# Kernel optimization log

Hardware: AMD Instinct MI355X
Metric: run time of the kernel (lower is better)

## Reference

```python
import jax, jax.numpy as jnp
import numpy as np

H = 64          # hidden_dim
EP = 60000      # edges per relation type; block order: nmos, pmos, R, L, C
E = 5 * EP
N_IN = 50000
N_OUT = 50000


def _gelu(x):
    return jax.nn.gelu(x, approximate=False)  # torch nn.GELU default = exact erf


def _mlp_blocked(x, Ws, bs):
    # x: [T, N, Din]; independent MLP per relation-type block; GELU after all but last layer
    for i, (W, b) in enumerate(zip(Ws, bs)):
        x = jnp.einsum('tnd,tdh->tnh', x, W) + b[:, None, :]
        if i < len(Ws) - 1:
            x = _gelu(x)
    return x


def _mlp(x, Ws, bs):
    for i, (W, b) in enumerate(zip(Ws, bs)):
        x = x @ W + b
        if i < len(Ws) - 1:
            x = _gelu(x)
    return x


def _segment_softmax(logits, seg, num_seg):
    # torch_geometric-style softmax: normalized per dst-node segment, per feature column
    m = jax.ops.segment_max(logits, seg, num_segments=num_seg)
    ex = jnp.exp(logits - m[seg])
    den = jax.ops.segment_sum(ex, seg, num_segments=num_seg)
    return ex / den[seg]


def _forward(floats, src_types, dst_types, src_nodes, dst_nodes,
             vg_types, vg_idx, vb_types, vb_idx, n_output_nodes):
    (input_voltages, device_params, nf1_W, nf1_b,
     ef1_W1, ef1_b1, ef1_W2, ef1_b2, ef1_W3, ef1_b3,
     ef2m_W1, ef2m_b1, ef2m_W2, ef2m_b2, ef2m_W3, ef2m_b3, ef2m_W4, ef2m_b4,
     ef2r_W1, ef2r_b1, ef2r_W2, ef2r_b2, ef2r_W3, ef2r_b3, ef2r_W4, ef2r_b4,
     self_W1, self_b1, self_W2, self_b2, self_W3, self_b3, self_W4, self_b4,
     score_W, score_b) = floats
    # ef1: per-relation-type 3-layer MLP on the scalar device parameter -> [E, H]
    ef1 = _mlp_blocked(device_params,
                       [ef1_W1, ef1_W2, ef1_W3],
                       [ef1_b1, ef1_b2, ef1_b3]).reshape(E, H)
    nf1_input = input_voltages[:, None] @ nf1_W + nf1_b           # [N_IN, H]
    # (ef1 @ ef1.T)[dst_out] @ ef1 == ef1[dst_out] @ (ef1.T @ ef1) -- avoids the E x E matrix
    logits = ef1 @ (ef1.T @ ef1)                                  # [E, H]
    # edges whose dst is not an 'output' node go to a dump segment that is dropped
    seg = jnp.where(dst_types == 1, dst_nodes, n_output_nodes)
    att = _segment_softmax(logits, seg, n_output_nodes + 1)
    nf1_output = jax.ops.segment_sum(att * ef1, seg,
                                     num_segments=n_output_nodes + 1)[:n_output_nodes]

    def pick(types, idx):
        # node_types.index: 0 -> 'input' table, 1 -> 'output' table
        return jnp.where((types == 0)[:, None], nf1_input[idx], nf1_output[idx])

    nf1_src = pick(src_types, src_nodes)
    nf1_dst = pick(dst_types, dst_nodes)
    nf1_vg = pick(vg_types, vg_idx)     # gate node feats (mos edges only) [2*EP, H]
    nf1_vb = pick(vb_types, vb_idx)     # bulk node feats (mos edges only) [2*EP, H]

    M = 2 * EP
    x_mos = jnp.concatenate([ef1[:M], nf1_src[:M], nf1_dst[:M], nf1_vg, nf1_vb], -1).reshape(2, EP, 5 * H)
    x_rlc = jnp.concatenate([ef1[M:], nf1_src[M:], nf1_dst[M:]], -1).reshape(3, EP, 3 * H)
    ef2_mos = _mlp_blocked(x_mos, [ef2m_W1, ef2m_W2, ef2m_W3, ef2m_W4],
                           [ef2m_b1, ef2m_b2, ef2m_b3, ef2m_b4])
    ef2_rlc = _mlp_blocked(x_rlc, [ef2r_W1, ef2r_W2, ef2r_W3, ef2r_W4],
                           [ef2r_b1, ef2r_b2, ef2r_b3, ef2r_b4])
    ef2 = jnp.concatenate([ef2_mos.reshape(M, H), ef2_rlc.reshape(3 * EP, H)], 0)
    ef2 = ef2 + _mlp(ef1, [self_W1, self_W2, self_W3, self_W4],
                     [self_b1, self_b2, self_b3, self_b4])
    return ef2 @ score_W + score_b                                # [E, H]


def setup_inputs():
    key = jax.random.key(0)
    ks = iter(jax.random.split(key, 64))

    def nrm(shape, s):
        return jax.random.normal(next(ks), shape, jnp.float32) * s

    def ri(shape, hi):
        return jax.random.randint(next(ks), shape, 0, hi, jnp.int32)

    w = 0.1  # ~ xavier-normal scale for these fan-ins
    return {
        'input_voltages': nrm([N_IN], 1.0),
        'device_params': nrm([5, EP, 1], 1.0),
        'src_types': ri([E], 2), 'dst_types': ri([E], 2),
        'src_nodes': ri([E], N_IN), 'dst_nodes': ri([E], N_OUT),
        'vg_types': ri([2 * EP], 2), 'vg_idx': ri([2 * EP], N_IN),
        'vb_types': ri([2 * EP], 2), 'vb_idx': ri([2 * EP], N_IN),
        'n_output_nodes': N_OUT,
        'nf1_W': nrm([1, H], w), 'nf1_b': nrm([H], w),
        'ef1_W1': nrm([5, 1, H], w), 'ef1_b1': nrm([5, H], w),
        'ef1_W2': nrm([5, H, H], w), 'ef1_b2': nrm([5, H], w),
        'ef1_W3': nrm([5, H, H], w), 'ef1_b3': nrm([5, H], w),
        'ef2m_W1': nrm([2, 5 * H, H], 0.05), 'ef2m_b1': nrm([2, H], w),
        'ef2m_W2': nrm([2, H, H], w), 'ef2m_b2': nrm([2, H], w),
        'ef2m_W3': nrm([2, H, H], w), 'ef2m_b3': nrm([2, H], w),
        'ef2m_W4': nrm([2, H, H], w), 'ef2m_b4': nrm([2, H], w),
        'ef2r_W1': nrm([3, 3 * H, H], 0.05), 'ef2r_b1': nrm([3, H], w),
        'ef2r_W2': nrm([3, H, H], w), 'ef2r_b2': nrm([3, H], w),
        'ef2r_W3': nrm([3, H, H], w), 'ef2r_b3': nrm([3, H], w),
        'ef2r_W4': nrm([3, H, H], w), 'ef2r_b4': nrm([3, H], w),
        'self_W1': nrm([H, H], w), 'self_b1': nrm([H], w),
        'self_W2': nrm([H, H], w), 'self_b2': nrm([H], w),
        'self_W3': nrm([H, H], w), 'self_b3': nrm([H], w),
        'self_W4': nrm([H, H], w), 'self_b4': nrm([H], w),
        'score_W': nrm([H, H], w), 'score_b': nrm([H], w),
    }


def reference(input_voltages, device_params, src_types, dst_types, src_nodes, dst_nodes,
              vg_types, vg_idx, vb_types, vb_idx, n_output_nodes,
              nf1_W, nf1_b,
              ef1_W1, ef1_b1, ef1_W2, ef1_b2, ef1_W3, ef1_b3,
              ef2m_W1, ef2m_b1, ef2m_W2, ef2m_b2, ef2m_W3, ef2m_b3, ef2m_W4, ef2m_b4,
              ef2r_W1, ef2r_b1, ef2r_W2, ef2r_b2, ef2r_W3, ef2r_b3, ef2r_W4, ef2r_b4,
              self_W1, self_b1, self_W2, self_b2, self_W3, self_b3, self_W4, self_b4,
              score_W, score_b):
    floats = (input_voltages, device_params, nf1_W, nf1_b,
              ef1_W1, ef1_b1, ef1_W2, ef1_b2, ef1_W3, ef1_b3,
              ef2m_W1, ef2m_b1, ef2m_W2, ef2m_b2, ef2m_W3, ef2m_b3, ef2m_W4, ef2m_b4,
              ef2r_W1, ef2r_b1, ef2r_W2, ef2r_b2, ef2r_W3, ef2r_b3, ef2r_W4, ef2r_b4,
              self_W1, self_b1, self_W2, self_b2, self_W3, self_b3, self_W4, self_b4,
              score_W, score_b)
    return _forward(floats, src_types, dst_types, src_nodes, dst_nodes,
                    vg_types, vg_idx, vb_types, vb_idx, n_output_nodes)
```

## Files before the change

kernel.cpp:

```cpp
#include <hip/hip_runtime.h>
#include <hip/hip_bf16.h>

#define EP 60000
#define NE 300000
#define M2 120000
#define NIN 50000
#define NOUT 50000
#define PAD 65
#define NIMG 49

typedef __bf16 b16x8 __attribute__((ext_vector_type(8)));
typedef float f32x4 __attribute__((ext_vector_type(4)));
typedef unsigned short us8 __attribute__((ext_vector_type(8)));
typedef unsigned short us4 __attribute__((ext_vector_type(4)));

__device__ __forceinline__ float gelu_f(float x) {
    return 0.5f * x * (1.0f + erff(x * 0.70710678118654752440f));
}

__device__ __forceinline__ float gelu_fast(float x) {
    float ax = fabsf(x) * 0.70710678118654752440f;
    float t = __builtin_amdgcn_rcpf(fmaf(0.3275911f, ax, 1.0f));
    float y = fmaf(fmaf(fmaf(fmaf(1.061405429f, t, -1.453152027f), t, 1.421413741f),
                        t, -0.284496736f), t, 0.254829592f) * t;
    float e = __expf(-ax * ax);
    float erf = fmaf(-y, e, 1.0f);
    return 0.5f * x * (1.0f + copysignf(erf, x));
}

__device__ __forceinline__ unsigned short bfhi(float f) {
    unsigned int u = __float_as_uint(f);
    u += 0x7FFFu + ((u >> 16) & 1u);
    return (unsigned short)(u >> 16);
}

__device__ __forceinline__ void split2(float f, unsigned short& h, unsigned short& l) {
    h = bfhi(f);
    float fh = __uint_as_float(((unsigned int)h) << 16);
    l = bfhi(f - fh);
}

__device__ __forceinline__ void split2f(float f, unsigned short& h, unsigned short& l) {
    unsigned int u = __float_as_uint(f);
    h = (unsigned short)(u >> 16);
    float fh = __uint_as_float(u & 0xFFFF0000u);
    l = bfhi(f - fh);
}

__device__ __forceinline__ float bf2f(unsigned short u) {
    return __uint_as_float(((unsigned int)u) << 16);
}

__device__ __forceinline__ int xidx(int row, int col) {
    return (row * 64 + col) ^ ((row & 7) << 3);
}

__device__ __forceinline__ b16x8 ldfrag(const unsigned short* p, int id) {
    return __builtin_bit_cast(b16x8, *(const us8*)(p + id));
}

__device__ __forceinline__ f32x4 MF(b16x8 a, b16x8 b, f32x4 c) {
    return __builtin_amdgcn_mfma_f32_16x16x32_bf16(a, b, c, 0, 0, 0);
}

__device__ __forceinline__ void zacc(f32x4 a[2][2]) {
#pragma unroll
    for (int i = 0; i < 2; ++i)
#pragma unroll
        for (int j = 0; j < 2; ++j) a[i][j] = (f32x4){0.f, 0.f, 0.f, 0.f};
}

__device__ __forceinline__ void gll16(const unsigned short* g, unsigned short* l) {
    __builtin_amdgcn_global_load_lds((const __attribute__((address_space(1))) void*)g,
                                     (__attribute__((address_space(3))) void*)l, 16, 0, 0);
}

__device__ __forceinline__ void stageWimg(const unsigned short* __restrict__ img,
                                          unsigned short* __restrict__ WHL, int tid) {
    int w = tid >> 6, lane = tid & 63;
#pragma unroll
    for (int j = 0; j < 2; ++j)
        gll16(img + w * 1024 + j * 512 + lane * 8, WHL + w * 1024 + j * 512);
}

__device__ __forceinline__ void stageX_rows(const unsigned short* __restrict__ src, int rmax,
                                            unsigned short* __restrict__ XH, unsigned short* __restrict__ XL,
                                            int tid) {
#pragma unroll
    for (int q = 0; q < 4; ++q) {
        int f = q * 512 + tid;
        int row = f >> 4, cc = f & 15;
        int rc = min(row, rmax - 1);
        us8 v = *(const us8*)(src + (size_t)rc * 128 + cc * 8);
        unsigned short* pl = (cc < 8) ? XH : XL;
        *(us8*)(pl + xidx(row, (cc & 7) * 8)) = v;
    }
}

__device__ __forceinline__ void stageX_pick(const int* __restrict__ tp, const int* __restrict__ ix, int base,
                                            int rmax, const float* __restrict__ volt,
                                            const unsigned short* __restrict__ nfo,
                                            const float* __restrict__ sNW, const float* __restrict__ sNB,
                                            unsigned short* __restrict__ XH, unsigned short* __restrict__ XL,
                                            int tid) {
#pragma unroll
    for (int q = 0; q < 4; ++q) {
        int f = q * 512 + tid;
        int row = f >> 4, cc = f & 15;
        int rc = min(row, rmax - 1);
        int ty = tp[base + rc];
        int idx = ix[base + rc];
        int c8 = (cc & 7) * 8;
        unsigned short* pl = (cc < 8) ? XH : XL;
        us8 v;
        if (ty == 0) {
            float vv = volt[idx];
#pragma unroll
            for (int j = 0; j < 8; ++j) {
                float x = fmaf(vv, sNW[c8 + j], sNB[c8 + j]);
                unsigned short h, l;
                split2f(x, h, l);
                v[j] = (cc < 8) ? h : l;
            }
        } else {
            v = *(const us8*)(nfo + (size_t)idx * 128 + cc * 8);
        }
        *(us8*)(pl + xidx(row, c8)) = v;
    }
}

__device__ __forceinline__ void mf_gemm64(const unsigned short* __restrict__ XH, const unsigned short* __restrict__ XL,
                                          const unsigned short* __restrict__ WH, const unsigned short* __restrict__ WL,
                                          f32x4 acc[2][2], int wr, int wc, int lane) {
    int lr = lane & 15, g = lane >> 4;
#pragma unroll
    for (int kk = 0; kk < 2; ++kk) {
        int k0 = kk * 32 + g * 8;
        b16x8 ah[2], al[2];
#pragma unroll
        for (int rt = 0; rt < 2; ++rt) {
            int id = xidx(wr * 32 + rt * 16 + lr, k0);
            ah[rt] = ldfrag(XH, id);
            al[rt] = ldfrag(XL, id);
        }
#pragma unroll
        for (int t = 0; t < 2; ++t) {
            int id = xidx((wc * 2 + t) * 16 + lr, k0);
            b16x8 bh = ldfrag(WH, id), bl = ldfrag(WL, id);
#pragma unroll
            for (int rt = 0; rt < 2; ++rt) {
                acc[rt][t] = MF(ah[rt], bh, acc[rt][t]);
                acc[rt][t] = MF(ah[rt], bl, acc[rt][t]);
                acc[rt][t] = MF(al[rt], bh, acc[rt][t]);
            }
        }
    }
}

template <bool GELU, bool FAST>
__device__ __forceinline__ void writeback(f32x4 acc[2][2], const float* __restrict__ sb,
                                          unsigned short* __restrict__ XH, unsigned short* __restrict__ XL,
                                          int wr, int wc, int lane) {
    int lr = lane & 15, g = lane >> 4;
#pragma unroll
    for (int rt = 0; rt < 2; ++rt)
#pragma unroll
        for (int t = 0; t < 2; ++t)
#pragma unroll
            for (int r = 0; r < 4; ++r) {
                int row = wr * 32 + rt * 16 + g * 4 + r;
                int col = (wc * 2 + t) * 16 + lr;
                float v = acc[rt][t][r] + sb[col];
                if (GELU) v = FAST ? gelu_fast(v) : gelu_f(v);
                unsigned short h, l;
                if (FAST) split2f(v, h, l); else split2(v, h, l);
                int id = xidx(row, col);
                XH[id] = h; XL[id] = l;
            }
}

__device__ __forceinline__ void writeglob_nt(f32x4 acc[2][2], const float* __restrict__ sb,
                                             float* __restrict__ dst, int rmax, int wr, int wc, int lane) {
    int lr = lane & 15, g = lane >> 4;
#pragma unroll
    for (int rt = 0; rt < 2; ++rt)
#pragma unroll
        for (int t = 0; t < 2; ++t)
#pragma unroll
            for (int r = 0; r < 4; ++r) {
                int row = wr * 32 + rt * 16 + g * 4 + r;
                if (row < rmax) {
                    int col = (wc * 2 + t) * 16 + lr;
                    __builtin_nontemporal_store(acc[rt][t][r] + sb[col], &dst[(size_t)row * 64 + col]);
                }
            }
}

__device__ __forceinline__ void writeglob_split(f32x4 acc[2][2], const float* __restrict__ sb,
                                                unsigned short* __restrict__ dst, int rmax,
                                                int wr, int wc, int lane) {
    int lr = lane & 15, g = lane >> 4;
#pragma unroll
    for (int rt = 0; rt < 2; ++rt)
#pragma unroll
        for (int t = 0; t < 2; ++t)
#pragma unroll
            for (int r = 0; r < 4; ++r) {
                int row = wr * 32 + rt * 16 + g * 4 + r;
                if (row < rmax) {
                    int col = (wc * 2 + t) * 16 + lr;
                    float v = acc[rt][t][r] + sb[col];
                    unsigned short h, l;
                    split2(v, h, l);
                    dst[(size_t)row * 128 + col] = h;
                    dst[(size_t)row * 128 + 64 + col] = l;
                }
            }
}

__global__ void k_zero(int* __restrict__ p, int n) {
    int i = blockIdx.x * 256 + threadIdx.x;
    if (i < n) p[i] = 0;
}

__global__ __launch_bounds__(256) void k_prepw(
    const float* __restrict__ e1W2, const float* __restrict__ e1W3,
    const float* __restrict__ mW1, const float* __restrict__ mW2,
    const float* __restrict__ mW3, const float* __restrict__ mW4,
    const float* __restrict__ rW1, const float* __restrict__ rW2,
    const float* __restrict__ rW3, const float* __restrict__ rW4,
    const float* __restrict__ sw1, const float* __restrict__ sw2,
    const float* __restrict__ sw3, const float* __restrict__ sw4,
    const float* __restrict__ scw, unsigned short* __restrict__ wimg) {
    int b = blockIdx.x, tid = threadIdx.x;
    const float* src;
    if (b < 5) src = e1W2 + b * 4096;
    else if (b < 10) src = e1W3 + (b - 5) * 4096;
    else if (b < 20) src = mW1 + (b - 10) * 4096;
    else if (b < 22) src = mW2 + (b - 20) * 4096;
    else if (b < 24) src = mW3 + (b - 22) * 4096;
    else if (b < 26) src = mW4 + (b - 24) * 4096;
    else if (b < 35) src = rW1 + (b - 26) * 4096;
    else if (b < 38) src = rW2 + (b - 35) * 4096;
    else if (b < 41) src = rW3 + (b - 38) * 4096;
    else if (b < 44) src = rW4 + (b - 41) * 4096;
    else if (b == 44) src = sw1;
    else if (b == 45) src = sw2;
    else if (b == 46) src = sw3;
    else if (b == 47) src = sw4;
    else src = scw;
    unsigned short* dst = wimg + (size_t)b * 8192;
#pragma unroll
    for (int q = 0; q < 4; ++q) {
        int flat = q * 256 + tid;
        int k = flat >> 4, n4 = (flat & 15) * 4;
        float4 v = ((const float4*)src)[flat];
        float vv[4] = {v.x, v.y, v.z, v.w};
#pragma unroll
        for (int i = 0; i < 4; ++i) {
            unsigned short h, l;
            split2(vv[i], h, l);
            int id = xidx(n4 + i, k);
            dst[id] = h;
            dst[4096 + id] = l;
        }
    }
}

__global__ __launch_bounds__(512, 4) void k_ef1(
    const float* __restrict__ dp,
    const float* __restrict__ w1, const float* __restrict__ b1,
    const float* __restrict__ b2, const float* __restrict__ b3,
    const unsigned short* __restrict__ wimg,
    unsigned short* __restrict__ e1s) {
    __shared__ unsigned short XH[8192], XL[8192], WHL[8192];
    __shared__ float sb[2][64], sW1[64], sB1[64];
    const int tid = threadIdx.x, ty = blockIdx.y;
    const int i0 = blockIdx.x * 128;
    const int rmax = min(128, EP - i0);
    const int w = tid >> 6, lane = tid & 63;
    const int wr = w >> 1, wc = w & 1;
    const size_t row0 = (size_t)ty * EP + i0;

    stageWimg(wimg + (size_t)ty * 8192, WHL, tid);
    if (tid < 64) { sW1[tid] = w1[ty * 64 + tid]; sB1[tid] = b1[ty * 64 + tid]; }
    else if (tid < 128) sb[0][tid - 64] = b2[ty * 64 + tid - 64];
    else if (tid < 192) sb[1][tid - 128] = b3[ty * 64 + tid - 128];
    __syncthreads();
#pragma unroll
    for (int q = 0; q < 4; ++q) {
        int flat = q * 512 + tid;
        int rr = flat >> 4, cc = flat & 15;
        int rc = min(rr, rmax - 1);
        float d = dp[(size_t)ty * EP + i0 + rc];
        us4 h, l;
#pragma unroll
        for (int j = 0; j < 4; ++j) {
            int c = cc * 4 + j;
            float v = gelu_f(fmaf(d, sW1[c], sB1[c]));
            unsigned short hh, ll;
            split2(v, hh, ll);
            h[j] = hh; l[j] = ll;
        }
        *(us4*)(XH + xidx(rr, cc * 4)) = h;
        *(us4*)(XL + xidx(rr, cc * 4)) = l;
    }
    __syncthreads();
    f32x4 acc[2][2];
    zacc(acc); mf_gemm64(XH, XL, WHL, WHL + 4096, acc, wr, wc, lane);
    __syncthreads();
    writeback<true, false>(acc, sb[0], XH, XL, wr, wc, lane);
    stageWimg(wimg + (size_t)(5 + ty) * 8192, WHL, tid);
    __syncthreads();
    zacc(acc); mf_gemm64(XH, XL, WHL, WHL + 4096, acc, wr, wc, lane);
    writeglob_split(acc, sb[1], e1s + row0 * 128, rmax, wr, wc, lane);
}

__device__ __forceinline__ void zero16(float* a) {
#pragma unroll
    for (int q = 0; q < 16; ++q) a[q] = 0.f;
}

__device__ __forceinline__ void stage4k(const float* __restrict__ g, float* __restrict__ l) {
    const float4* g4 = (const float4*)g;
    float4* l4 = (float4*)l;
    int t = threadIdx.x;
#pragma unroll
    for (int q = 0; q < 4; ++q) l4[q * 256 + t] = g4[q * 256 + t];
}

__device__ __forceinline__ void tile_gemm(const float* __restrict__ xt, const float* __restrict__ Wl,
                                          float* __restrict__ acc, int r, int c4) {
    const float4* W4 = (const float4*)Wl;
#pragma unroll 8
    for (int k = 0; k < 64; ++k) {
        float xv = xt[r * PAD + k];
#pragma unroll
        for (int q = 0; q < 4; ++q) {
            float4 w = W4[k * 16 + c4 + q];
            acc[q * 4 + 0] = fmaf(xv, w.x, acc[q * 4 + 0]);
            acc[q * 4 + 1] = fmaf(xv, w.y, acc[q * 4 + 1]);
            acc[q * 4 + 2] = fmaf(xv, w.z, acc[q * 4 + 2]);
            acc[q * 4 + 3] = fmaf(xv, w.w, acc[q * 4 + 3]);
        }
    }
}

__global__ __launch_bounds__(256) void k_gram(const unsigned short* __restrict__ e1s, float* __restrict__ G) {
    __shared__ float4 rows[512];
    const int tid = threadIdx.x;
    const int i = tid >> 4, j = tid & 15;
    float4 accs[4];
#pragma unroll
    for (int p = 0; p < 4; ++p) accs[p] = make_float4(0, 0, 0, 0);
    int nb = gridDim.x;
    int per = (NE + nb - 1) / nb;
    int r0 = blockIdx.x * per;
    int r1 = min(r0 + per, NE);
    for (int rb = r0; rb < r1; rb += 32) {
        __syncthreads();
#pragma unroll
        for (int q = 0; q < 2; ++q) {
            int f = q * 256 + tid;
            int row = rb + (f >> 4), ch = f & 15;
            if (row < r1) {
                const unsigned short* rp = e1s + (size_t)row * 128;
                us4 h = *(const us4*)(rp + ch * 4);
                us4 l = *(const us4*)(rp + 64 + ch * 4);
                rows[f] = make_float4(bf2f(h[0]) + bf2f(l[0]), bf2f(h[1]) + bf2f(l[1]),
                                      bf2f(h[2]) + bf2f(l[2]), bf2f(h[3]) + bf2f(l[3]));
            } else {
                rows[f] = make_float4(0, 0, 0, 0);
            }
        }
        __syncthreads();
#pragma unroll 4
        for (int rr = 0; rr < 32; ++rr) {
            float4 a = rows[rr * 16 + i];
            float4 b = rows[rr * 16 + j];
            float ap[4] = {a.x, a.y, a.z, a.w};
#pragma unroll
            for (int p = 0; p < 4; ++p) {
                accs[p].x = fmaf(ap[p], b.x, accs[p].x);
                accs[p].y = fmaf(ap[p], b.y, accs[p].y);
                accs[p].z = fmaf(ap[p], b.z, accs[p].z);
                accs[p].w = fmaf(ap[p], b.w, accs[p].w);
            }
        }
    }
#pragma unroll
    for (int p = 0; p < 4; ++p) {
        int row = (i * 4 + p) * 64 + j * 4;
        atomicAdd(&G[row + 0], accs[p].x);
        atomicAdd(&G[row + 1], accs[p].y);
        atomicAdd(&G[row + 2], accs[p].z);
        atomicAdd(&G[row + 3], accs[p].w);
    }
}

__global__ void k_hist(const int* __restrict__ dst_t, const int* __restrict__ dst_n, int* __restrict__ hist) {
    int e = blockIdx.x * 256 + threadIdx.x;
    if (e < NE && dst_t[e] == 1) atomicAdd(&hist[dst_n[e]], 1);
}

__global__ __launch_bounds__(1024) void k_scan(const int* __restrict__ hist, int* __restrict__ row_start) {
    __shared__ int part[1024];
    const int tid = threadIdx.x;
    const int chunk = (NOUT + 1023) / 1024;
    int lo = tid * chunk, hi = min(lo + chunk, NOUT);
    int s = 0;
    for (int i = lo; i < hi; ++i) s += hist[i];
    part[tid] = s;
    __syncthreads();
    for (int off = 1; off < 1024; off <<= 1) {
        int v = part[tid];
        int add = (tid >= off) ? part[tid - off] : 0;
        __syncthreads();
        part[tid] = v + add;
        __syncthreads();
    }
    int base = (tid == 0) ? 0 : part[tid - 1];
    for (int i = lo; i < hi; ++i) { row_start[i] = base; base += hist[i]; }
    if (lo < NOUT && hi == NOUT) row_start[NOUT] = base;
}

__global__ void k_scatter(const int* __restrict__ dst_t, const int* __restrict__ dst_n,
                          const int* __restrict__ row_start, int* __restrict__ cursor, int* __restrict__ elist) {
    int e = blockIdx.x * 256 + threadIdx.x;
    if (e < NE && dst_t[e] == 1) {
        int n = dst_n[e];
        int pos = atomicAdd(&cursor[n], 1);
        elist[row_start[n] + pos] = e;
    }
}

__global__ __launch_bounds__(256) void k_logits_c(const unsigned short* __restrict__ e1s,
                                                  const float* __restrict__ G,
                                                  const int* __restrict__ row_start,
                                                  const int* __restrict__ elist,
                                                  float* __restrict__ lgc) {
    __shared__ float A[64 * PAD], Wb[4096];
    const int tid = threadIdx.x;
    const int NV = row_start[NOUT];
    const int i0 = blockIdx.x * 64;
    if (i0 >= NV) return;
    const int rmax = min(64, NV - i0);
    const int r = tid & 63, c0 = (tid >> 6) * 16, c4 = c0 >> 2;
    stage4k(G, Wb);
#pragma unroll
    for (int q = 0; q < 4; ++q) {
        int flat = q * 256 + tid;
        int rr = flat >> 4, cc = flat & 15;
        int rc = min(rr, rmax - 1);
        int eid = elist[i0 + rc];
        const unsigned short* rp = e1s + (size_t)eid * 128;
        us4 h = *(const us4*)(rp + cc * 4);
        us4 l = *(const us4*)(rp + 64 + cc * 4);
        float* d = &A[rr * PAD + cc * 4];
#pragma unroll
        for (int j = 0; j < 4; ++j) d[j] = bf2f(h[j]) + bf2f(l[j]);
    }
    __syncthreads();
    float acc[16];
    zero16(acc); tile_gemm(A, Wb, acc, r, c4);
    if (r < rmax) {
        float* dst = lgc + (size_t)(i0 + r) * 64;
#pragma unroll
        for (int q = 0; q < 4; ++q)
            ((float4*)dst)[c4 + q] =
                make_float4(acc[q * 4 + 0], acc[q * 4 + 1], acc[q * 4 + 2], acc[q * 4 + 3]);
    }
}

__global__ __launch_bounds__(256) void k_att(const float* __restrict__ lgc, const unsigned short* __restrict__ e1s,
                                             const int* __restrict__ row_start, const int* __restrict__ elist,
                                             unsigned short* __restrict__ nfo) {
    int n = blockIdx.x * 4 + (threadIdx.x >> 6);
    int lane = threadIdx.x & 63;
    if (n >= NOUT) return;
    int s = row_start[n], t = row_start[n + 1];
    float m = -3.0e38f, den = 0.f, num = 0.f;
    for (int i = s; i < t; ++i) {
        int eid = elist[i];
        float x = lgc[(size_t)i * 64 + lane];
        float e = bf2f(e1s[(size_t)eid * 128 + lane]) + bf2f(e1s[(size_t)eid * 128 + 64 + lane]);
        float mn = fmaxf(m, x);
        float sc = __expf(m - mn);
        float ex = __expf(x - mn);
        den = fmaf(den, sc, ex);
        num = fmaf(num, sc, ex * e);
        m = mn;
    }
    float v = (t > s) ? num / den : 0.f;
    unsigned short h, l;
    split2(v, h, l);
    nfo[(size_t)n * 128 + lane] = h;
    nfo[(size_t)n * 128 + 64 + lane] = l;
}

__global__ __launch_bounds__(512, 4) void k_fuse(
    const unsigned short* __restrict__ e1s, const unsigned short* __restrict__ nfo,
    const unsigned short* __restrict__ wimg, const float* __restrict__ volt,
    const int* __restrict__ src_t, const int* __restrict__ src_n,
    const int* __restrict__ dst_t, const int* __restrict__ dst_n,
    const int* __restrict__ vg_t, const int* __restrict__ vg_i,
    const int* __restrict__ vb_t, const int* __restrict__ vb_i,
    const float* __restrict__ nf1W, const float* __restrict__ nf1b,
    const float* __restrict__ mb1, const float* __restrict__ mb2,
    const float* __restrict__ mb3, const float* __restrict__ mb4,
    const float* __restrict__ rb1, const float* __restrict__ rb2,
    const float* __restrict__ rb3, const float* __restrict__ rb4,
    const float* __restrict__ selb1, const float* __restrict__ selb2,
    const float* __restrict__ selb3, const float* __restrict__ selb4,
    const float* __restrict__ scb, float* __restrict__ out) {
    __shared__ unsigned short XH[8192], XL[8192], WHL[8192];
    __shared__ float sb[3][64], sNW[64], sNB[64];
    const int tid = threadIdx.x;
    const int gy = blockIdx.y;
    const bool mos = gy < 2;
    const int ty = mos ? gy : gy - 2;
    const int nch = mos ? 5 : 3;
    const int i0 = blockIdx.x * 128;
    const int rmax = min(128, EP - i0);
    const int w = tid >> 6, lane = tid & 63;
    const int wr = w >> 1, wc = w & 1;
    const int lr = lane & 15;
    const int erow0 = (mos ? 0 : M2) + ty * EP + i0;
    const int w1base = mos ? 10 + ty * 5 : 26 + ty * 3;
    const int w2img = mos ? 20 + ty : 35 + ty;
    const int w3img = mos ? 22 + ty : 38 + ty;
    const int w4img = mos ? 24 + ty : 41 + ty;
    const float* b1 = mos ? mb1 : rb1;
    const float* b2 = mos ? mb2 : rb2;
    const float* b3 = mos ? mb3 : rb3;
    const float* b4 = mos ? mb4 : rb4;

    stageWimg(wimg + (size_t)44 * 8192, WHL, tid);
    stageX_rows(e1s + (size_t)erow0 * 128, rmax, XH, XL, tid);
    if (tid < 64) sNW[tid] = nf1W[tid];
    else if (tid < 128) sNB[tid - 64] = nf1b[tid - 64];
    else if (tid < 192) sb[0][tid - 128] = b1[ty * 64 + tid - 128];
    __syncthreads();

    f32x4 acc[2][2], accS[2][2], ef2r[2][2];
    zacc(accS);
    mf_gemm64(XH, XL, WHL, WHL + 4096, accS, wr, wc, lane);
    __syncthreads();
    stageWimg(wimg + (size_t)w1base * 8192, WHL, tid);
    __syncthreads();
    zacc(acc);
    mf_gemm64(XH, XL, WHL, WHL + 4096, acc, wr, wc, lane);
    for (int c = 1; c < nch; ++c) {
        __syncthreads();
        stageWimg(wimg + (size_t)(w1base + c) * 8192, WHL, tid);
        if (c == 1) stageX_pick(src_t, src_n, erow0, rmax, volt, nfo, sNW, sNB, XH, XL, tid);
        else if (c == 2) stageX_pick(dst_t, dst_n, erow0, rmax, volt, nfo, sNW, sNB, XH, XL, tid);
        else if (c == 3) stageX_pick(vg_t, vg_i, erow0, rmax, volt, nfo, sNW, sNB, XH, XL, tid);
        else stageX_pick(vb_t, vb_i, erow0, rmax, volt, nfo, sNW, sNB, XH, XL, tid);
        __syncthreads();
        mf_gemm64(XH, XL, WHL, WHL + 4096, acc, wr, wc, lane);
    }
    __syncthreads();
    writeback<true, true>(acc, sb[0], XH, XL, wr, wc, lane);
    stageWimg(wimg + (size_t)w2img * 8192, WHL, tid);
    if (tid < 64) sb[1][tid] = b2[ty * 64 + tid];
    __syncthreads();
    zacc(acc); mf_gemm64(XH, XL, WHL, WHL + 4096, acc, wr, wc, lane);
    __syncthreads();
    writeback<true, true>(acc, sb[1], XH, XL, wr, wc, lane);
    stageWimg(wimg + (size_t)w3img * 8192, WHL, tid);
    if (tid < 64) sb[2][tid] = b3[ty * 64 + tid];
    __syncthreads();
    zacc(acc); mf_gemm64(XH, XL, WHL, WHL + 4096, acc, wr, wc, lane);
    __syncthreads();
    writeback<true, true>(acc, sb[2], XH, XL, wr, wc, lane);
    stageWimg(wimg + (size_t)w4img * 8192, WHL, tid);
    if (tid < 64) sb[0][tid] = b4[ty * 64 + tid];
    else if (tid < 128) sb[1][tid - 64] = selb1[tid - 64];
    __syncthreads();
    zacc(acc); mf_gemm64(XH, XL, WHL, WHL + 4096, acc, wr, wc, lane);
#pragma unroll
    for (int rt = 0; rt < 2; ++rt)
#pragma unroll
        for (int t = 0; t < 2; ++t)
#pragma unroll
            for (int r = 0; r < 4; ++r)
                ef2r[rt][t][r] = acc[rt][t][r] + sb[0][(wc * 2 + t) * 16 + lr];
    __syncthreads();
    writeback<true, true>(accS, sb[1], XH, XL, wr, wc, lane);
    stageWimg(wimg + (size_t)45 * 8192, WHL, tid);
    if (tid < 64) sb[2][tid] = selb2[tid];
    __syncthreads();
    zacc(acc); mf_gemm64(XH, XL, WHL, WHL + 4096, acc, wr, wc, lane);
    __syncthreads();
    writeback<true, true>(acc, sb[2], XH, XL, wr, wc, lane);
    stageWimg(wimg + (size_t)46 * 8192, WHL, tid);
    if (tid < 64) sb[0][tid] = selb3[tid];
    __syncthreads();
    zacc(acc); mf_gemm64(XH, XL, WHL, WHL + 4096, acc, wr, wc, lane);
    __syncthreads();
    writeback<true, true>(acc, sb[0], XH, XL, wr, wc, lane);
    stageWimg(wimg + (size_t)47 * 8192, WHL, tid);
    if (tid < 64) sb[1][tid] = selb4[tid];
    __syncthreads();
    zacc(acc); mf_gemm64(XH, XL, WHL, WHL + 4096, acc, wr, wc, lane);
    __syncthreads();
    {
        int g = lane >> 4;
#pragma unroll
        for (int rt = 0; rt < 2; ++rt)
#pragma unroll
            for (int t = 0; t < 2; ++t)
#pragma unroll
                for (int r = 0; r < 4; ++r) {
                    int row = wr * 32 + rt * 16 + g * 4 + r;
                    int col = (wc * 2 + t) * 16 + lr;
                    float v = acc[rt][t][r] + sb[1][col] + ef2r[rt][t][r];
                    unsigned short h, l;
                    split2f(v, h, l);
                    int id = xidx(row, col);
                    XH[id] = h; XL[id] = l;
                }
    }
    stageWimg(wimg + (size_t)48 * 8192, WHL, tid);
    if (tid < 64) sb[2][tid] = scb[tid];
    __syncthreads();
    zacc(acc); mf_gemm64(XH, XL, WHL, WHL + 4096, acc, wr, wc, lane);
    writeglob_nt(acc, sb[2], out + (size_t)erow0 * 64, rmax, wr, wc, lane);
}

extern "C" void kernel_launch(void* const* d_in, const int* in_sizes, int n_in,
                              void* d_out, int out_size, void* d_ws, size_t ws_size,
                              hipStream_t stream) {
    const float* volt = (const float*)d_in[0];
    const float* dp   = (const float*)d_in[1];
    const int* src_t  = (const int*)d_in[2];
    const int* dst_t  = (const int*)d_in[3];
    const int* src_n  = (const int*)d_in[4];
    const int* dst_n  = (const int*)d_in[5];
    const int* vg_t   = (const int*)d_in[6];
    const int* vg_i   = (const int*)d_in[7];
    const int* vb_t   = (const int*)d_in[8];
    const int* vb_i   = (const int*)d_in[9];
    const float* nf1W = (const float*)d_in[11];
    const float* nf1b = (const float*)d_in[12];
    const float* e1W1 = (const float*)d_in[13];
    const float* e1b1 = (const float*)d_in[14];
    const float* e1W2 = (const float*)d_in[15];
    const float* e1b2 = (const float*)d_in[16];
    const float* e1W3 = (const float*)d_in[17];
    const float* e1b3 = (const float*)d_in[18];
    const float* mW1 = (const float*)d_in[19];  const float* mb1 = (const float*)d_in[20];
    const float* mW2 = (const float*)d_in[21];  const float* mb2 = (const float*)d_in[22];
    const float* mW3 = (const float*)d_in[23];  const float* mb3 = (const float*)d_in[24];
    const float* mW4 = (const float*)d_in[25];  const float* mb4 = (const float*)d_in[26];
    const float* rW1 = (const float*)d_in[27];  const float* rb1 = (const float*)d_in[28];
    const float* rW2 = (const float*)d_in[29];  const float* rb2 = (const float*)d_in[30];
    const float* rW3 = (const float*)d_in[31];  const float* rb3 = (const float*)d_in[32];
    const float* rW4 = (const float*)d_in[33];  const float* rb4 = (const float*)d_in[34];
    const float* selW1 = (const float*)d_in[35]; const float* selb1 = (const float*)d_in[36];
    const float* selW2 = (const float*)d_in[37]; const float* selb2 = (const float*)d_in[38];
    const float* selW3 = (const float*)d_in[39]; const float* selb3 = (const float*)d_in[40];
    const float* selW4 = (const float*)d_in[41]; const float* selb4 = (const float*)d_in[42];
    const float* scW = (const float*)d_in[43];   const float* scb = (const float*)d_in[44];

    float* lgc = (float*)d_ws;
    unsigned short* NFO  = (unsigned short*)(lgc + (size_t)NE * 64);
    unsigned short* WIMG = NFO + (size_t)NOUT * 128;
    float* G = (float*)(WIMG + (size_t)NIMG * 8192);
    int* hist      = (int*)(G + 4096);
    int* cursor    = hist + NOUT;
    int* row_start = cursor + NOUT;
    int* elist     = row_start + NOUT + 1;
    unsigned short* E1S = (unsigned short*)d_out;

    const int T128_EP = (EP + 127) / 128;
    const int TILES_E = (NE + 63) / 64;
    dim3 b256(256), b512(512);

    k_prepw<<<NIMG, b256, 0, stream>>>(e1W2, e1W3, mW1, mW2, mW3, mW4,
                                       rW1, rW2, rW3, rW4, selW1, selW2, selW3, selW4, scW, WIMG);
    {
        int nz = 4096 + NOUT + NOUT;
        k_zero<<<(nz + 255) / 256, b256, 0, stream>>>((int*)G, nz);
    }
    k_ef1<<<dim3(T128_EP, 5), b512, 0, stream>>>(dp, e1W1, e1b1, e1b2, e1b3, WIMG, E1S);
    k_hist<<<(NE + 255) / 256, b256, 0, stream>>>(dst_t, dst_n, hist);
    k_scan<<<1, 1024, 0, stream>>>(hist, row_start);
    k_scatter<<<(NE + 255) / 256, b256, 0, stream>>>(dst_t, dst_n, row_start, cursor, elist);
    k_gram<<<640, b256, 0, stream>>>(E1S, G);
    k_logits_c<<<TILES_E, b256, 0, stream>>>(E1S, G, row_start, elist, lgc);
    k_att<<<NOUT / 4, b256, 0, stream>>>(lgc, E1S, row_start, elist, NFO);
    k_fuse<<<dim3(T128_EP, 5), b512, 0, stream>>>(E1S, NFO, WIMG, volt,
        src_t, src_n, dst_t, dst_n, vg_t, vg_i, vb_t, vb_i, nf1W, nf1b,
        mb1, mb2, mb3, mb4, rb1, rb2, rb3, rb4,
        selb1, selb2, selb3, selb4, scb, (float*)d_out);
}
```

Measured before the change: 479.6 us.

## Fuse logits GEMV into attention kernel, drop logits buffer and nontemporal stores

Removes the separate k_logits_c kernel, which materialized a [E,64] fp32 logits buffer. k_att now stages the 64x64 Gram matrix in LDS and computes each edge's logit row on the fly per wave, using a per-wave LDS row and an FMA loop over k. This avoids writing and re-reading the large logits buffer and saves a launch, at the cost of serial per-edge GEMV latency inside the softmax loop and an extra 16KB G load per block. The final output store also switches from nontemporal to regular stores.

```diff
diff --git a/kernel.cpp b/kernel.cpp
--- a/kernel.cpp
+++ b/kernel.cpp
@@ -179,8 +179,8 @@
             }
 }
 
-__device__ __forceinline__ void writeglob_nt(f32x4 acc[2][2], const float* __restrict__ sb,
-                                             float* __restrict__ dst, int rmax, int wr, int wc, int lane) {
+__device__ __forceinline__ void writeglob(f32x4 acc[2][2], const float* __restrict__ sb,
+                                          float* __restrict__ dst, int rmax, int wr, int wc, int lane) {
     int lr = lane & 15, g = lane >> 4;
 #pragma unroll
     for (int rt = 0; rt < 2; ++rt)
@@ -191,7 +191,7 @@
                 int row = wr * 32 + rt * 16 + g * 4 + r;
                 if (row < rmax) {
                     int col = (wc * 2 + t) * 16 + lr;
-                    __builtin_nontemporal_store(acc[rt][t][r] + sb[col], &dst[(size_t)row * 64 + col]);
+                    dst[(size_t)row * 64 + col] = acc[rt][t][r] + sb[col];
                 }
             }
 }
@@ -321,31 +321,6 @@
     for (int q = 0; q < 16; ++q) a[q] = 0.f;
 }
 
-__device__ __forceinline__ void stage4k(const float* __restrict__ g, float* __restrict__ l) {
-    const float4* g4 = (const float4*)g;
-    float4* l4 = (float4*)l;
-    int t = threadIdx.x;
-#pragma unroll
-    for (int q = 0; q < 4; ++q) l4[q * 256 + t] = g4[q * 256 + t];
-}
-
-__device__ __forceinline__ void tile_gemm(const float* __restrict__ xt, const float* __restrict__ Wl,
-                                          float* __restrict__ acc, int r, int c4) {
-    const float4* W4 = (const float4*)Wl;
-#pragma unroll 8
-    for (int k = 0; k < 64; ++k) {
-        float xv = xt[r * PAD + k];
-#pragma unroll
-        for (int q = 0; q < 4; ++q) {
-            float4 w = W4[k * 16 + c4 + q];
-            acc[q * 4 + 0] = fmaf(xv, w.x, acc[q * 4 + 0]);
-            acc[q * 4 + 1] = fmaf(xv, w.y, acc[q * 4 + 1]);
-            acc[q * 4 + 2] = fmaf(xv, w.z, acc[q * 4 + 2]);
-            acc[q * 4 + 3] = fmaf(xv, w.w, acc[q * 4 + 3]);
-        }
-    }
-}
-
 __global__ __launch_bounds__(256) void k_gram(const unsigned short* __restrict__ e1s, float* __restrict__ G) {
     __shared__ float4 rows[512];
     const int tid = threadIdx.x;
@@ -434,62 +409,42 @@
     }
 }
 
-__global__ __launch_bounds__(256) void k_logits_c(const unsigned short* __restrict__ e1s,
-                                                  const float* __restrict__ G,
-                                                  const int* __restrict__ row_start,
-                                                  const int* __restrict__ elist,
-                                                  float* __restrict__ lgc) {
-    __shared__ float A[64 * PAD], Wb[4096];
+__global__ __launch_bounds__(256) void k_att(const unsigned short* __restrict__ e1s,
+                                             const float* __restrict__ G,
+                                             const int* __restrict__ row_start,
+                                             const int* __restrict__ elist,
+                                             unsigned short* __restrict__ nfo) {
+    __shared__ float sG[4096];
+    __shared__ float xrow[4][64];
     const int tid = threadIdx.x;
-    const int NV = row_start[NOUT];
-    const int i0 = blockIdx.x * 64;
-    if (i0 >= NV) return;
-    const int rmax = min(64, NV - i0);
-    const int r = tid & 63, c0 = (tid >> 6) * 16, c4 = c0 >> 2;
-    stage4k(G, Wb);
-#pragma unroll
-    for (int q = 0; q < 4; ++q) {
-        int flat = q * 256 + tid;
-        int rr = flat >> 4, cc = flat & 15;
-        int rc = min(rr, rmax - 1);
-        int eid = elist[i0 + rc];
-        const unsigned short* rp = e1s + (size_t)eid * 128;
-        us4 h = *(const us4*)(rp + cc * 4);
-        us4 l = *(const us4*)(rp + 64 + cc * 4);
-        float* d = &A[rr * PAD + cc * 4];
-#pragma unroll
-        for (int j = 0; j < 4; ++j) d[j] = bf2f(h[j]) + bf2f(l[j]);
-    }
-    __syncthreads();
-    float acc[16];
-    zero16(acc); tile_gemm(A, Wb, acc, r, c4);
-    if (r < rmax) {
-        float* dst = lgc + (size_t)(i0 + r) * 64;
-#pragma unroll
-        for (int q = 0; q < 4; ++q)
-            ((float4*)dst)[c4 + q] =
-                make_float4(acc[q * 4 + 0], acc[q * 4 + 1], acc[q * 4 + 2], acc[q * 4 + 3]);
-    }
-}
-
-__global__ __launch_bounds__(256) void k_att(const float* __restrict__ lgc, const unsigned short* __restrict__ e1s,
-                                             const int* __restrict__ row_start, const int* __restrict__ elist,
-                                             unsigned short* __restrict__ nfo) {
-    int n = blockIdx.x * 4 + (threadIdx.x >> 6);
-    int lane = threadIdx.x & 63;
+    {
+        const float4* g4 = (const float4*)G;
+        float4* l4 = (float4*)sG;
+#pragma unroll
+        for (int q = 0; q < 4; ++q) l4[q * 256 + tid] = g4[q * 256 + tid];
+    }
+    __syncthreads();
+    const int wv = tid >> 6, lane = tid & 63;
+    int n = blockIdx.x * 4 + wv;
     if (n >= NOUT) return;
     int s = row_start[n], t = row_start[n + 1];
     float m = -3.0e38f, den = 0.f, num = 0.f;
     for (int i = s; i < t; ++i) {
         int eid = elist[i];
-        float x = lgc[(size_t)i * 64 + lane];
         float e = bf2f(e1s[(size_t)eid * 128 + lane]) + bf2f(e1s[(size_t)eid * 128 + 64 + lane]);
-        float mn = fmaxf(m, x);
+        xrow[wv][lane] = e;
+        __builtin_amdgcn_wave_barrier();
+        float lg = 0.f;
+#pragma unroll 8
+        for (int k = 0; k < 64; ++k)
+            lg = fmaf(xrow[wv][k], sG[k * 64 + lane], lg);
+        float mn = fmaxf(m, lg);
         float sc = __expf(m - mn);
-        float ex = __expf(x - mn);
+        float ex = __expf(lg - mn);
         den = fmaf(den, sc, ex);
         num = fmaf(num, sc, ex * e);
         m = mn;
+        __builtin_amdgcn_wave_barrier();
     }
     float v = (t > s) ? num / den : 0.f;
     unsigned short h, l;
@@ -626,7 +581,7 @@
     if (tid < 64) sb[2][tid] = scb[tid];
     __syncthreads();
     zacc(acc); mf_gemm64(XH, XL, WHL, WHL + 4096, acc, wr, wc, lane);
-    writeglob_nt(acc, sb[2], out + (size_t)erow0 * 64, rmax, wr, wc, lane);
+    writeglob(acc, sb[2], out + (size_t)erow0 * 64, rmax, wr, wc, lane);
 }
 
 extern "C" void kernel_launch(void* const* d_in, const int* in_sizes, int n_in,
@@ -664,8 +619,7 @@
     const float* selW4 = (const float*)d_in[41]; const float* selb4 = (const float*)d_in[42];
     const float* scW = (const float*)d_in[43];   const float* scb = (const float*)d_in[44];
 
-    float* lgc = (float*)d_ws;
-    unsigned short* NFO  = (unsigned short*)(lgc + (size_t)NE * 64);
+    unsigned short* NFO  = (unsigned short*)d_ws;
     unsigned short* WIMG = NFO + (size_t)NOUT * 128;
     float* G = (float*)(WIMG + (size_t)NIMG * 8192);
     int* hist      = (int*)(G + 4096);
@@ -675,7 +629,6 @@
     unsigned short* E1S = (unsigned short*)d_out;
 
     const int T128_EP = (EP + 127) / 128;
-    const int TILES_E = (NE + 63) / 64;
     dim3 b256(256), b512(512);
 
     k_prepw<<<NIMG, b256, 0, stream>>>(e1W2, e1W3, mW1, mW2, mW3, mW4,
@@ -689,8 +642,7 @@
     k_scan<<<1, 1024, 0, stream>>>(hist, row_start);
     k_scatter<<<(NE + 255) / 256, b256, 0, stream>>>(dst_t, dst_n, row_start, cursor, elist);
     k_gram<<<640, b256, 0, stream>>>(E1S, G);
-    k_logits_c<<<TILES_E, b256, 0, stream>>>(E1S, G, row_start, elist, lgc);
-    k_att<<<NOUT / 4, b256, 0, stream>>>(lgc, E1S, row_start, elist, NFO);
+    k_att<<<NOUT / 4, b256, 0, stream>>>(E1S, G, row_start, elist, NFO);
     k_fuse<<<dim3(T128_EP, 5), b512, 0, stream>>>(E1S, NFO, WIMG, volt,
         src_t, src_n, dst_t, dst_n, vg_t, vg_i, vb_t, vb_i, nf1W, nf1b,
         mb1, mb2, mb3, mb4, rb1, rb2, rb3, rb4,
```

Measured after the change: 490.7 us. 2.3% more time.

## Compute Gram matrix with split-bf16 MFMA and use plain stores for output

Applied to the files above, without the earlier changes.

The Gram kernel (ef1^T ef1 over 300k edges) moves from scalar FP32 FMAs to bf16 MFMA. Each value is split into high and low bf16 parts and three cross products (hh, hl, lh) are accumulated to stay close to FP32 accuracy. Each chunk is transposed into padded LDS tiles so the reduction runs along the edge dimension, and the grid now strides over 64-row chunks. Separately, the final output write switches from nontemporal to normal stores. Costs are the LDS transpose-scatter overhead and a small precision loss from dropping the lo*lo term.

```diff
diff --git a/kernel.cpp b/kernel.cpp
--- a/kernel.cpp
+++ b/kernel.cpp
@@ -8,6 +8,7 @@
 #define NOUT 50000
 #define PAD 65
 #define NIMG 49
+#define GP 72
 
 typedef __bf16 b16x8 __attribute__((ext_vector_type(8)));
 typedef float f32x4 __attribute__((ext_vector_type(4)));
@@ -179,8 +180,8 @@
             }
 }
 
-__device__ __forceinline__ void writeglob_nt(f32x4 acc[2][2], const float* __restrict__ sb,
-                                             float* __restrict__ dst, int rmax, int wr, int wc, int lane) {
+__device__ __forceinline__ void writeglob(f32x4 acc[2][2], const float* __restrict__ sb,
+                                          float* __restrict__ dst, int rmax, int wr, int wc, int lane) {
     int lr = lane & 15, g = lane >> 4;
 #pragma unroll
     for (int rt = 0; rt < 2; ++rt)
@@ -191,7 +192,7 @@
                 int row = wr * 32 + rt * 16 + g * 4 + r;
                 if (row < rmax) {
                     int col = (wc * 2 + t) * 16 + lr;
-                    __builtin_nontemporal_store(acc[rt][t][r] + sb[col], &dst[(size_t)row * 64 + col]);
+                    dst[(size_t)row * 64 + col] = acc[rt][t][r] + sb[col];
                 }
             }
 }
@@ -347,55 +348,53 @@
 }
 
 __global__ __launch_bounds__(256) void k_gram(const unsigned short* __restrict__ e1s, float* __restrict__ G) {
-    __shared__ float4 rows[512];
+    __shared__ unsigned short TH[64 * GP], TL[64 * GP];
     const int tid = threadIdx.x;
-    const int i = tid >> 4, j = tid & 15;
-    float4 accs[4];
-#pragma unroll
-    for (int p = 0; p < 4; ++p) accs[p] = make_float4(0, 0, 0, 0);
-    int nb = gridDim.x;
-    int per = (NE + nb - 1) / nb;
-    int r0 = blockIdx.x * per;
-    int r1 = min(r0 + per, NE);
-    for (int rb = r0; rb < r1; rb += 32) {
+    const int wv = tid >> 6, lane = tid & 63;
+    const int lr = lane & 15, g = lane >> 4;
+    f32x4 acc[4];
+#pragma unroll
+    for (int t = 0; t < 4; ++t) acc[t] = (f32x4){0.f, 0.f, 0.f, 0.f};
+    const int nchk = (NE + 63) >> 6;
+    for (int ch = blockIdx.x; ch < nchk; ch += gridDim.x) {
+        int r0 = ch * 64;
         __syncthreads();
 #pragma unroll
-        for (int q = 0; q < 2; ++q) {
+        for (int q = 0; q < 4; ++q) {
             int f = q * 256 + tid;
-            int row = rb + (f >> 4), ch = f & 15;
-            if (row < r1) {
-                const unsigned short* rp = e1s + (size_t)row * 128;
-                us4 h = *(const us4*)(rp + ch * 4);
-                us4 l = *(const us4*)(rp + 64 + ch * 4);
-                rows[f] = make_float4(bf2f(h[0]) + bf2f(l[0]), bf2f(h[1]) + bf2f(l[1]),
-                                      bf2f(h[2]) + bf2f(l[2]), bf2f(h[3]) + bf2f(l[3]));
-            } else {
-                rows[f] = make_float4(0, 0, 0, 0);
+            int pl = f >> 9, rem = f & 511;
+            int row = rem >> 3, cc = rem & 7;
+            int rr = r0 + row;
+            us8 v = (us8){0, 0, 0, 0, 0, 0, 0, 0};
+            if (rr < NE) v = *(const us8*)(e1s + (size_t)rr * 128 + pl * 64 + cc * 8);
+            unsigned short* dstp = pl ? TL : TH;
+#pragma unroll
+            for (int j = 0; j < 8; ++j) dstp[(cc * 8 + j) * GP + row] = v[j];
+        }
+        __syncthreads();
+#pragma unroll
+        for (int kk = 0; kk < 2; ++kk) {
+            int k0 = kk * 32 + g * 8;
+            b16x8 ah = ldfrag(TH, (wv * 16 + lr) * GP + k0);
+            b16x8 al = ldfrag(TL, (wv * 16 + lr) * GP + k0);
+#pragma unroll
+            for (int b = 0; b < 4; ++b) {
+                b16x8 bh = ldfrag(TH, (b * 16 + lr) * GP + k0);
+                b16x8 bl = ldfrag(TL, (b * 16 + lr) * GP + k0);
+                acc[b] = MF(ah, bh, acc[b]);
+                acc[b] = MF(ah, bl, acc[b]);
+                acc[b] = MF(al, bh, acc[b]);
             }
         }
-        __syncthreads();
-#pragma unroll 4
-        for (int rr = 0; rr < 32; ++rr) {
-            float4 a = rows[rr * 16 + i];
-            float4 b = rows[rr * 16 + j];
-            float ap[4] = {a.x, a.y, a.z, a.w};
-#pragma unroll
-            for (int p = 0; p < 4; ++p) {
-                accs[p].x = fmaf(ap[p], b.x, accs[p].x);
-                accs[p].y = fmaf(ap[p], b.y, accs[p].y);
-                accs[p].z = fmaf(ap[p], b.z, accs[p].z);
-                accs[p].w = fmaf(ap[p], b.w, accs[p].w);
-            }
-        }
-    }
-#pragma unroll
-    for (int p = 0; p < 4; ++p) {
-        int row = (i * 4 + p) * 64 + j * 4;
-        atomicAdd(&G[row + 0], accs[p].x);
-        atomicAdd(&G[row + 1], accs[p].y);
-        atomicAdd(&G[row + 2], accs[p].z);
-        atomicAdd(&G[row + 3], accs[p].w);
-    }
+    }
+#pragma unroll
+    for (int b = 0; b < 4; ++b)
+#pragma unroll
+        for (int r = 0; r < 4; ++r) {
+            int row = wv * 16 + g * 4 + r;
+            int col = b * 16 + lr;
+            atomicAdd(&G[row * 64 + col], acc[b][r]);
+        }
 }
 
 __global__ void k_hist(const int* __restrict__ dst_t, const int* __restrict__ dst_n, int* __restrict__ hist) {
@@ -626,7 +625,7 @@
     if (tid < 64) sb[2][tid] = scb[tid];
     __syncthreads();
     zacc(acc); mf_gemm64(XH, XL, WHL, WHL + 4096, acc, wr, wc, lane);
-    writeglob_nt(acc, sb[2], out + (size_t)erow0 * 64, rmax, wr, wc, lane);
+    writeglob(acc, sb[2], out + (size_t)erow0 * 64, rmax, wr, wc, lane);
 }
 
 extern "C" void kernel_launch(void* const* d_in, const int* in_sizes, int n_in,
```

After: 414.1 us. 1.16x faster.
